# Kernel optimization log

Hardware: AMD Instinct MI355X
Metric: run time of the kernel (lower is better)

The kernel has to match this reference:

```python
import jax, jax.numpy as jnp
import numpy as np

EPS_CLAMP = 1e-6
TAU2 = 1.0


def _l2norm_rows(x):
    # F.normalize(x, p=2, dim=1) with eps=1e-12
    n = jnp.sqrt(jnp.sum(x * x, axis=1, keepdims=True))
    return x / jnp.maximum(n, 1e-12)


def _ws_v22(x_mean, x_std):
    m = _l2norm_rows(x_mean)                      # [N, F]
    c = _l2norm_rows(jnp.exp(x_std))              # [N, F]
    sq = jnp.sum(m * m, axis=1)                   # [N]
    # squared euclidean pairwise distance (cdist(...)**2)
    d2 = jnp.maximum(sq[:, None] + sq[None, :] - 2.0 * (m @ m.T), 0.0)
    csum = jnp.sum(c, axis=1)                     # [N]
    cs = jnp.sqrt(c)
    res = d2 + csum[:, None] + csum[None, :] - 2.0 * (cs @ cs.T)
    return jnp.exp(-res)                          # [N, N]


def _gcn_conv_dense(A, x, W, b):
    # PyG GCNConv with dense weighted adjacency A (A[i,j] = weight of edge i->j),
    # add_remaining_self_loops(fill=1), deg over target (column sums),
    # norm_ij = d_i^-1/2 * A_ij * d_j^-1/2, aggregate at target: out = A_norm^T @ (xW) + b
    diag = jnp.diagonal(A)
    A = A + jnp.diag(jnp.where(diag > 0, 0.0, 1.0))  # add self-loop weight 1 only where missing
    deg = jnp.sum(A, axis=0)                         # column sums (target degree)
    dis = jnp.where(deg > 0, deg ** -0.5, 0.0)
    An = dis[:, None] * A * dis[None, :]
    return An.T @ (x @ W) + b


def _encoder(A, x, W0, b0, W1, b1):
    h = jax.nn.relu(_gcn_conv_dense(A, x, W0, b0))
    return jax.nn.relu(_gcn_conv_dense(A, h, W1, b1))


def setup_inputs() -> dict:
    key = jax.random.key(0)
    ks = jax.random.split(key, 16)
    N, F, H = 4096, 512, 256
    s_in = 1.0 / np.sqrt(F)
    s_h = 1.0 / np.sqrt(2 * H)
    inp = {
        "x": jax.random.normal(ks[0], (N, F), dtype=jnp.float32),
        "new_edge": jax.random.uniform(ks[1], (N, N), dtype=jnp.float32),
        "beta": jax.random.uniform(ks[2], (1,), dtype=jnp.float32),
        "delta": jax.random.uniform(ks[3], (1,), dtype=jnp.float32),
        "eps": jax.random.uniform(ks[4], (N, N), dtype=jnp.float32),
        "Wm": jax.random.uniform(ks[5], (F, F), jnp.float32, -s_in, s_in),
        "bm": jax.random.uniform(ks[6], (F,), jnp.float32, -s_in, s_in),
        "Ws": jax.random.uniform(ks[7], (F, F), jnp.float32, -s_in, s_in),
        "bs": jax.random.uniform(ks[8], (F,), jnp.float32, -s_in, s_in),
        "mW0": jax.random.uniform(ks[9], (F, 2 * H), jnp.float32, -s_in, s_in) ,
        "mb0": jnp.zeros((2 * H,), jnp.float32),
        "mW1": jax.random.uniform(ks[10], (2 * H, H), jnp.float32, -s_h, s_h),
        "mb1": jnp.zeros((H,), jnp.float32),
        "sW0": jax.random.uniform(ks[11], (F, 2 * H), jnp.float32, -s_in, s_in),
        "sb0": jnp.zeros((2 * H,), jnp.float32),
        "sW1": jax.random.uniform(ks[12], (2 * H, H), jnp.float32, -s_h, s_h),
        "sb1": jnp.zeros((H,), jnp.float32),
    }
    return inp


def reference(x, new_edge, beta, delta, eps, Wm, bm, Ws, bs,
              mW0, mb0, mW1, mb1, sW0, sb0, sW1, sb1):
    b = beta[0]
    d = delta[0]
    x_mean = x @ Wm + bm
    x_std = x @ Ws + bs
    ws = _l2norm_rows(_ws_v22(x_mean, x_std))       # F.normalize(WS_v22(...)) row-wise
    term = (1.0 - b) * ws + b * new_edge
    term = jnp.clip(term, EPS_CLAMP, 1.0 - EPS_CLAMP)
    term = jnp.log(term / (1.0 - term))
    e = jnp.clip(eps, EPS_CLAMP, 1.0 - EPS_CLAMP)
    term = term + jnp.log(e / (1.0 - e))
    term = jax.nn.sigmoid(term / TAU2)
    term = jnp.where(term > d, term, 0.0)           # dense sparsified adjacency
    z_mean = _encoder(term, x_mean, mW0, mb0, mW1, mb1)
    z_std = _encoder(term, x_std, sW0, sb0, sW1, sb1)
    return z_mean, z_std
```

## Files before the change

### kernel.cpp

```cpp
#include <hip/hip_runtime.h>
#include <cstddef>

static constexpr int kN = 4096;
static constexpr int kF = 512;
static constexpr int kH = 256;
static constexpr float kClamp = 1e-6f;

using bf16x8 = __attribute__((ext_vector_type(8))) __bf16;
using f32x4 = __attribute__((ext_vector_type(4))) float;
using ushort8 = __attribute__((ext_vector_type(8))) unsigned short;
using ushort4v = __attribute__((ext_vector_type(4))) unsigned short;

static constexpr size_t PLANE_XF = (size_t)kN * kF;
static constexpr size_t PLANE_NN = (size_t)kN * kN;
static constexpr size_t PLANE_W = (size_t)512 * 512;
static constexpr size_t PLANE_W1 = (size_t)256 * 512;
static constexpr size_t PLANE_V0 = (size_t)1024 * kN;
static constexpr size_t PLANE_H = (size_t)kN * 1024;
static constexpr size_t PLANE_V1 = (size_t)512 * kN;

__device__ __forceinline__ unsigned short f2bf(float x) {
  unsigned int u = __float_as_uint(x);
  u += 0x7fffu + ((u >> 16) & 1u);
  return (unsigned short)(u >> 16);
}
__device__ __forceinline__ float bf2f(unsigned short h) {
  return __uint_as_float(((unsigned int)h) << 16);
}
__device__ __forceinline__ void split3(float x, unsigned short& h,
                                       unsigned short& m, unsigned short& l) {
  h = f2bf(x);
  const float r1 = x - bf2f(h);
  m = f2bf(r1);
  l = f2bf(r1 - bf2f(m));
}
__device__ __forceinline__ void split2(float x, unsigned short& h,
                                       unsigned short& m) {
  h = f2bf(x);
  m = f2bf(x - bf2f(h));
}
__device__ __forceinline__ void split2x4(const float4 v, ushort4v& h4,
                                         ushort4v& m4) {
  unsigned short h, m;
  split2(v.x, h, m); h4.x = h; m4.x = m;
  split2(v.y, h, m); h4.y = h; m4.y = m;
  split2(v.z, h, m); h4.z = h; m4.z = m;
  split2(v.w, h, m); h4.w = h; m4.w = m;
}

__device__ __forceinline__ bf16x8 ldfrag(const unsigned short* p) {
  ushort8 r = *(const ushort8*)p;
  return __builtin_bit_cast(bf16x8, r);
}
__device__ __forceinline__ f32x4 mfma16(bf16x8 a, bf16x8 b, f32x4 c) {
  return __builtin_amdgcn_mfma_f32_16x16x32_bf16(a, b, c, 0, 0, 0);
}
__device__ __forceinline__ f32x4 mfma_split6(const bf16x8* a3, const bf16x8* b3,
                                             f32x4 acc) {
  acc = mfma16(a3[2], b3[0], acc);
  acc = mfma16(a3[0], b3[2], acc);
  acc = mfma16(a3[1], b3[1], acc);
  acc = mfma16(a3[1], b3[0], acc);
  acc = mfma16(a3[0], b3[1], acc);
  acc = mfma16(a3[0], b3[0], acc);
  return acc;
}

__device__ __forceinline__ void gload16(const unsigned short* g,
                                        unsigned short* l) {
  __builtin_amdgcn_global_load_lds(
      (const __attribute__((address_space(1))) void*)g,
      (__attribute__((address_space(3))) void*)l, 16, 0, 0);
}

__device__ __forceinline__ void tri_map(int b, int& bi, int& bj) {
  int x = (int)((sqrtf(8.0f * (float)b + 1.0f) - 1.0f) * 0.5f);
  while ((x + 1) * (x + 2) / 2 <= b) ++x;
  while (x * (x + 1) / 2 > b) --x;
  bi = x;
  bj = b - x * (x + 1) / 2;
}

__device__ __forceinline__ float block_reduce_sum(float v, float* sbuf) {
  const int tid = threadIdx.x;
  sbuf[tid] = v;
  __syncthreads();
#pragma unroll
  for (int s = 128; s > 0; s >>= 1) {
    if (tid < s) sbuf[tid] += sbuf[tid + s];
    __syncthreads();
  }
  const float r = sbuf[0];
  __syncthreads();
  return r;
}

__global__ __launch_bounds__(256) void prep_w(
    const float* s0, const float* s1, const float* s2, const float* s3,
    const float* s4, const float* s5, unsigned short* d0, unsigned short* d1,
    unsigned short* d2, unsigned short* d3, unsigned short* d4,
    unsigned short* d5) {
  const int seg = blockIdx.y;
  const float* src;
  unsigned short* dst;
  int N;
  bool tri;
  switch (seg) {
    case 0: src = s0; dst = d0; N = 512; tri = true; break;
    case 1: src = s1; dst = d1; N = 512; tri = true; break;
    case 2: src = s2; dst = d2; N = 512; tri = false; break;
    case 3: src = s3; dst = d3; N = 512; tri = false; break;
    case 4: src = s4; dst = d4; N = 256; tri = false; break;
    default: src = s5; dst = d5; N = 256; tri = false; break;
  }
  const int id = blockIdx.x * 256 + threadIdx.x;
  if (id >= 512 * N) return;
  const int k = id & 511;
  const int n = id >> 9;
  const float v = src[(size_t)k * N + n];
  const size_t base = (size_t)n * 512 + k;
  const size_t plane = (size_t)512 * N;
  if (tri) {
    unsigned short h, m, l;
    split3(v, h, m, l);
    dst[base] = h;
    dst[plane + base] = m;
    dst[2 * plane + base] = l;
  } else {
    unsigned short h, m;
    split2(v, h, m);
    dst[base] = h;
    dst[plane + base] = m;
  }
}

__global__ __launch_bounds__(256) void split_x(const float* __restrict__ x,
                                               unsigned short* __restrict__ x3) {
  const size_t id = (size_t)blockIdx.x * 256 + threadIdx.x;
  unsigned short h, m, l;
  split3(x[id], h, m, l);
  x3[id] = h;
  x3[PLANE_XF + id] = m;
  x3[2 * PLANE_XF + id] = l;
}

__global__ __launch_bounds__(256) void gemm_x(
    const unsigned short* __restrict__ A3, const unsigned short* __restrict__ B30,
    const unsigned short* __restrict__ B31, float* __restrict__ C0,
    float* __restrict__ C1, const float* __restrict__ bias0,
    const float* __restrict__ bias1) {
  constexpr int BM = 128, BN = 128, K = 512;
  __shared__ __align__(16) unsigned short Asl[3][BM][40];
  __shared__ __align__(16) unsigned short Bsl[3][BN][40];
  const int tid = threadIdx.x;
  const int lane = tid & 63;
  const int wave = tid >> 6;
  const int wm = wave >> 1, wn = wave & 1;
  const int m0 = blockIdx.y * BM;
  const int n0 = blockIdx.x * BN;
  const bool str1 = (n0 >= 512);
  const int nloc = str1 ? (n0 - 512) : n0;
  const unsigned short* Bb = str1 ? B31 : B30;
  const float* bias = str1 ? bias1 : bias0;
  float* C = str1 ? C1 : C0;
  const int rl = lane & 15;
  const int kq = (lane >> 4) * 8;
  const int q = lane >> 4;

  f32x4 acc[4][4];
#pragma unroll
  for (int i = 0; i < 4; ++i)
#pragma unroll
    for (int j = 0; j < 4; ++j) acc[i][j] = (f32x4){0.f, 0.f, 0.f, 0.f};

  for (int k0 = 0; k0 < K; k0 += 32) {
#pragma unroll
    for (int it = 0; it < 6; ++it) {
      const int c = tid + it * 256;
      const int plane = c >> 9;
      const int rem = c & 511;
      const int row = rem >> 2;
      const int kc = (rem & 3) * 8;
      const ushort8 v = *(const ushort8*)(&A3[(size_t)plane * PLANE_XF +
                                              (size_t)(m0 + row) * K + k0 + kc]);
      *(ushort8*)(&Asl[plane][row][kc]) = v;
    }
#pragma unroll
    for (int it = 0; it < 6; ++it) {
      const int c = tid + it * 256;
      const int plane = c >> 9;
      const int rem = c & 511;
      const int row = rem >> 2;
      const int kc = (rem & 3) * 8;
      const ushort8 v = *(const ushort8*)(&Bb[(size_t)plane * PLANE_W +
                                              (size_t)(nloc + row) * K + k0 + kc]);
      *(ushort8*)(&Bsl[plane][row][kc]) = v;
    }
    __syncthreads();
    bf16x8 af[4][3];
#pragma unroll
    for (int mt = 0; mt < 4; ++mt)
#pragma unroll
      for (int t = 0; t < 3; ++t)
        af[mt][t] = ldfrag(&Asl[t][wm * 64 + mt * 16 + rl][kq]);
#pragma unroll
    for (int nt = 0; nt < 4; ++nt) {
      bf16x8 b3[3];
#pragma unroll
      for (int t = 0; t < 3; ++t)
        b3[t] = ldfrag(&Bsl[t][wn * 64 + nt * 16 + rl][kq]);
#pragma unroll
      for (int mt = 0; mt < 4; ++mt)
        acc[mt][nt] = mfma_split6(af[mt], b3, acc[mt][nt]);
    }
    __syncthreads();
  }
#pragma unroll
  for (int mt = 0; mt < 4; ++mt)
#pragma unroll
    for (int nt = 0; nt < 4; ++nt) {
      const int col = nloc + wn * 64 + nt * 16 + rl;
      const int row0 = m0 + wm * 64 + mt * 16 + q * 4;
      const float bv = bias[col];
#pragma unroll
      for (int r = 0; r < 4; ++r)
        C[(size_t)(row0 + r) * 512 + col] = acc[mt][nt][r] + bv;
    }
}

template <int BM, int BN>
__global__ __launch_bounds__(256) void gemm2ct(
    const unsigned short* __restrict__ A0, const unsigned short* __restrict__ A1,
    int lda, size_t planeA, const unsigned short* __restrict__ B0,
    const unsigned short* __restrict__ B1, int ldb, size_t planeB,
    unsigned short* __restrict__ Cs0, unsigned short* __restrict__ Cs1, int ldc,
    size_t planeC, int N1, int K, const float* __restrict__ rowScale) {
  __shared__ __align__(16) unsigned short Asl[2][BM][40];
  __shared__ __align__(16) unsigned short Bsl[2][BN][40];
  const int tid = threadIdx.x;
  const int lane = tid & 63;
  const int wave = tid >> 6;
  const int wm = wave >> 1, wn = wave & 1;
  const int m0 = blockIdx.y * BM;
  const int n0 = blockIdx.x * BN;
  const bool str1 = (n0 >= N1);
  const int nloc = str1 ? (n0 - N1) : n0;
  const unsigned short* Ab = str1 ? A1 : A0;
  const unsigned short* Bb = str1 ? B1 : B0;
  const int rl = lane & 15;
  const int kq = (lane >> 4) * 8;
  const int q = lane >> 4;
  constexpr int MT = BM / 32;
  constexpr int NT = BN / 32;

  f32x4 acc[MT][NT];
#pragma unroll
  for (int i = 0; i < MT; ++i)
#pragma unroll
    for (int j = 0; j < NT; ++j) acc[i][j] = (f32x4){0.f, 0.f, 0.f, 0.f};

  for (int k0 = 0; k0 < K; k0 += 32) {
    constexpr int AIT = (2 * BM * 4) / 256;
#pragma unroll
    for (int it = 0; it < AIT; ++it) {
      const int c = tid + it * 256;
      const int plane = c / (BM * 4);
      const int rem = c % (BM * 4);
      const int row = rem >> 2;
      const int kc = (rem & 3) * 8;
      const ushort8 v = *(const ushort8*)(&Ab[(size_t)plane * planeA +
                                              (size_t)(m0 + row) * lda + k0 + kc]);
      *(ushort8*)(&Asl[plane][row][kc]) = v;
    }
    constexpr int BIT = (2 * BN * 4) / 256;
#pragma unroll
    for (int it = 0; it < BIT; ++it) {
      const int c = tid + it * 256;
      const int plane = c / (BN * 4);
      const int rem = c % (BN * 4);
      const int row = rem >> 2;
      const int kc = (rem & 3) * 8;
      const ushort8 v = *(const ushort8*)(&Bb[(size_t)plane * planeB +
                                              (size_t)(nloc + row) * ldb + k0 + kc]);
      *(ushort8*)(&Bsl[plane][row][kc]) = v;
    }
    __syncthreads();
    bf16x8 af[MT][2];
#pragma unroll
    for (int mt = 0; mt < MT; ++mt)
#pragma unroll
      for (int t = 0; t < 2; ++t)
        af[mt][t] = ldfrag(&Asl[t][wm * (BM / 2) + mt * 16 + rl][kq]);
#pragma unroll
    for (int nt = 0; nt < NT; ++nt) {
      const bf16x8 b0 = ldfrag(&Bsl[0][wn * (BN / 2) + nt * 16 + rl][kq]);
      const bf16x8 b1 = ldfrag(&Bsl[1][wn * (BN / 2) + nt * 16 + rl][kq]);
#pragma unroll
      for (int mt = 0; mt < MT; ++mt) {
        acc[mt][nt] = mfma16(af[mt][1], b0, acc[mt][nt]);
        acc[mt][nt] = mfma16(af[mt][0], b1, acc[mt][nt]);
        acc[mt][nt] = mfma16(af[mt][0], b0, acc[mt][nt]);
      }
    }
    __syncthreads();
  }

#pragma unroll
  for (int mt = 0; mt < MT; ++mt) {
#pragma unroll
    for (int nt = 0; nt < NT; ++nt) {
      const int colL = nloc + wn * (BN / 2) + nt * 16 + rl;
      const int row0 = m0 + wm * (BM / 2) + mt * 16 + q * 4;
      float4 v4;
      float* vp = &v4.x;
#pragma unroll
      for (int r = 0; r < 4; ++r) {
        float v = acc[mt][nt][r];
        if (rowScale) v *= rowScale[row0 + r];
        vp[r] = v;
      }
      unsigned short* C = str1 ? Cs1 : Cs0;
      ushort4v h4, m4;
      split2x4(v4, h4, m4);
      const size_t base = (size_t)colL * ldc + row0;
      *(ushort4v*)(&C[base]) = h4;
      *(ushort4v*)(&C[planeC + base]) = m4;
    }
  }
}

template <int BM, int BN, int GX, int GYP, int GZ>
__global__ __launch_bounds__(256) void gemm2k(
    const unsigned short* __restrict__ A, int lda, size_t planeA,
    const unsigned short* __restrict__ B, int ldb, size_t planeB,
    float* __restrict__ Cp, int ldc, int Mtot, int Ksl) {
  static_assert(BM == 128 && BN == 128, "DMA staging assumes 128x128");
  __shared__ __align__(16) unsigned short Asl[2][BM][32];
  __shared__ __align__(16) unsigned short Bsl[2][BN][32];
  const int lin = blockIdx.x;
  const int xcd = lin & 7;
  const int s = lin >> 3;
  constexpr int per = GX * GYP;
  const int z = s / per;
  const int r = s - z * per;
  const int bx = r % GX;
  const int by = xcd * GYP + r / GX;
  const int m0 = by * BM;
  const int n0 = bx * BN;
  const int kOff = z * Ksl;

  const int tid = threadIdx.x;
  const int lane = tid & 63;
  const int wave = tid >> 6;
  const int wm = wave >> 1, wn = wave & 1;
  const int rl = lane & 15;
  const int kq = (lane >> 4) * 8;
  const int q = lane >> 4;
  const int kqs = kq ^ (((rl >> 1) & 3) << 3);
  const int sslot = (((lane & 3) ^ ((lane >> 3) & 3)) * 8);
  constexpr int MT = BM / 32;
  constexpr int NT = BN / 32;

  f32x4 acc[MT][NT];
#pragma unroll
  for (int i = 0; i < MT; ++i)
#pragma unroll
    for (int j = 0; j < NT; ++j) acc[i][j] = (f32x4){0.f, 0.f, 0.f, 0.f};

  for (int k0 = 0; k0 < Ksl; k0 += 32) {
#pragma unroll
    for (int it = 0; it < 8; ++it) {
      const int c = it * 4 + wave;
      const bool isB = c >= 16;
      const int cl = isB ? (c - 16) : c;
      const int pl = cl >> 3;
      const int row = (cl & 7) * 16 + (lane >> 2);
      const unsigned short* src =
          (isB ? B + (size_t)pl * planeB + (size_t)(n0 + row) * ldb
               : A + (size_t)pl * planeA + (size_t)(m0 + row) * lda) +
          kOff + k0 + sslot;
      unsigned short* dst =
          (isB ? &Bsl[0][0][0] : &Asl[0][0][0]) + cl * 512 + 0;
      gload16(src, dst);
    }
    __syncthreads();
    bf16x8 af[MT][2];
#pragma unroll
    for (int mt = 0; mt < MT; ++mt)
#pragma unroll
      for (int t = 0; t < 2; ++t)
        af[mt][t] = ldfrag(&Asl[t][wm * (BM / 2) + mt * 16 + rl][kqs]);
#pragma unroll
    for (int nt = 0; nt < NT; ++nt) {
      const bf16x8 b0 = ldfrag(&Bsl[0][wn * (BN / 2) + nt * 16 + rl][kqs]);
      const bf16x8 b1 = ldfrag(&Bsl[1][wn * (BN / 2) + nt * 16 + rl][kqs]);
#pragma unroll
      for (int mt = 0; mt < MT; ++mt) {
        acc[mt][nt] = mfma16(af[mt][1], b0, acc[mt][nt]);
        acc[mt][nt] = mfma16(af[mt][0], b1, acc[mt][nt]);
        acc[mt][nt] = mfma16(af[mt][0], b0, acc[mt][nt]);
      }
    }
    __syncthreads();
  }

  const size_t zoff = (size_t)z * (size_t)Mtot * (size_t)ldc;
#pragma unroll
  for (int mt = 0; mt < MT; ++mt) {
#pragma unroll
    for (int nt = 0; nt < NT; ++nt) {
      const int colL = n0 + wn * (BN / 2) + nt * 16 + rl;
      const int row0 = m0 + wm * (BM / 2) + mt * 16 + q * 4;
#pragma unroll
      for (int r2 = 0; r2 < 4; ++r2)
        Cp[zoff + (size_t)(row0 + r2) * ldc + colL] = acc[mt][nt][r2];
    }
  }
}

__global__ __launch_bounds__(256) void row_stats(
    const float* __restrict__ XMf, const float* __restrict__ XSf,
    unsigned short* __restrict__ M2, unsigned short* __restrict__ CS2,
    unsigned short* __restrict__ XM2, unsigned short* __restrict__ XS2,
    float* __restrict__ sq, float* __restrict__ csum) {
  __shared__ float sbuf[256];
  const int i = blockIdx.x;
  const int tid = threadIdx.x;
  const size_t base = (size_t)i * kF;
  const size_t i0 = base + tid, i1 = base + tid + 256;
  const float x0 = XMf[i0], x1 = XMf[i1];
  {
    unsigned short h, m;
    split2(x0, h, m);
    XM2[i0] = h; XM2[PLANE_XF + i0] = m;
    split2(x1, h, m);
    XM2[i1] = h; XM2[PLANE_XF + i1] = m;
  }
  const float nrm = block_reduce_sum(x0 * x0 + x1 * x1, sbuf);
  const float inv = 1.0f / fmaxf(sqrtf(nrm), 1e-12f);
  const float m0 = x0 * inv, m1 = x1 * inv;
  {
    unsigned short h, m;
    split2(m0, h, m);
    M2[i0] = h; M2[PLANE_XF + i0] = m;
    split2(m1, h, m);
    M2[i1] = h; M2[PLANE_XF + i1] = m;
  }
  const float s2 = block_reduce_sum(m0 * m0 + m1 * m1, sbuf);
  if (tid == 0) sq[i] = s2;

  const float y0 = XSf[i0], y1 = XSf[i1];
  {
    unsigned short h, m;
    split2(y0, h, m);
    XS2[i0] = h; XS2[PLANE_XF + i0] = m;
    split2(y1, h, m);
    XS2[i1] = h; XS2[PLANE_XF + i1] = m;
  }
  const float e0 = expf(y0), e1 = expf(y1);
  const float nrm2 = block_reduce_sum(e0 * e0 + e1 * e1, sbuf);
  const float inv2 = 1.0f / fmaxf(sqrtf(nrm2), 1e-12f);
  const float c0 = e0 * inv2, c1 = e1 * inv2;
  const float sc = block_reduce_sum(c0 + c1, sbuf);
  if (tid == 0) csum[i] = sc;
  {
    unsigned short h, m;
    split2(sqrtf(c0), h, m);
    CS2[i0] = h; CS2[PLANE_XF + i0] = m;
    split2(sqrtf(c1), h, m);
    CS2[i1] = h; CS2[PLANE_XF + i1] = m;
  }
}

__global__ __launch_bounds__(256) void ws_mfma2(
    const unsigned short* __restrict__ M2, const unsigned short* __restrict__ CS2,
    const float* __restrict__ sq, const float* __restrict__ csum,
    float* __restrict__ WSR) {
  __shared__ __align__(16) unsigned short S[4][2][128][40];
  int bi, bj;
  tri_map(blockIdx.x, bi, bj);
  const int i0 = bi * 128, j0 = bj * 128;
  const int tid = threadIdx.x;
  const int lane = tid & 63;
  const int wave = tid >> 6;
  const int wm = wave >> 1, wn = wave & 1;
  const int rl = lane & 15;
  const int kq = (lane >> 4) * 8;
  const int q = lane >> 4;

  f32x4 aM[4][4], aC[4][4];
#pragma unroll
  for (int i = 0; i < 4; ++i)
#pragma unroll
    for (int j = 0; j < 4; ++j) {
      aM[i][j] = (f32x4){0.f, 0.f, 0.f, 0.f};
      aC[i][j] = (f32x4){0.f, 0.f, 0.f, 0.f};
    }

  for (int k0 = 0; k0 < kF; k0 += 32) {
#pragma unroll
    for (int it = 0; it < 16; ++it) {
      const int c = tid + it * 256;
      const int op = c >> 10;
      const int rem = c & 1023;
      const int plane = rem >> 9;
      const int r2 = rem & 511;
      const int row = r2 >> 2;
      const int kc = (r2 & 3) * 8;
      const unsigned short* mat = (op & 1) ? CS2 : M2;
      const int rowoff = (op < 2) ? i0 : j0;
      const ushort8 v = *(const ushort8*)(&mat[(size_t)plane * PLANE_XF +
                                               (size_t)(rowoff + row) * kF + k0 +
                                               kc]);
      *(ushort8*)(&S[op][plane][row][kc]) = v;
    }
    __syncthreads();
    bf16x8 am[4][2], ac[4][2];
#pragma unroll
    for (int mt = 0; mt < 4; ++mt)
#pragma unroll
      for (int t = 0; t < 2; ++t) {
        am[mt][t] = ldfrag(&S[0][t][wm * 64 + mt * 16 + rl][kq]);
        ac[mt][t] = ldfrag(&S[1][t][wm * 64 + mt * 16 + rl][kq]);
      }
#pragma unroll
    for (int nt = 0; nt < 4; ++nt) {
      const bf16x8 bm0 = ldfrag(&S[2][0][wn * 64 + nt * 16 + rl][kq]);
      const bf16x8 bm1 = ldfrag(&S[2][1][wn * 64 + nt * 16 + rl][kq]);
      const bf16x8 bc0 = ldfrag(&S[3][0][wn * 64 + nt * 16 + rl][kq]);
      const bf16x8 bc1 = ldfrag(&S[3][1][wn * 64 + nt * 16 + rl][kq]);
#pragma unroll
      for (int mt = 0; mt < 4; ++mt) {
        aM[mt][nt] = mfma16(am[mt][1], bm0, aM[mt][nt]);
        aM[mt][nt] = mfma16(am[mt][0], bm1, aM[mt][nt]);
        aM[mt][nt] = mfma16(am[mt][0], bm0, aM[mt][nt]);
        aC[mt][nt] = mfma16(ac[mt][1], bc0, aC[mt][nt]);
        aC[mt][nt] = mfma16(ac[mt][0], bc1, aC[mt][nt]);
        aC[mt][nt] = mfma16(ac[mt][0], bc0, aC[mt][nt]);
      }
    }
    __syncthreads();
  }

#pragma unroll
  for (int mt = 0; mt < 4; ++mt) {
#pragma unroll
    for (int nt = 0; nt < 4; ++nt) {
      const int j = j0 + wn * 64 + nt * 16 + rl;
      const int ib = i0 + wm * 64 + mt * 16 + q * 4;
      const float sqj = sq[j], csj = csum[j];
      float4 vv;
      float* vp = &vv.x;
#pragma unroll
      for (int r = 0; r < 4; ++r) {
        const int i = ib + r;
        const float d2 = fmaxf(sq[i] + sqj - 2.0f * aM[mt][nt][r], 0.0f);
        const float res = d2 + csum[i] + csj - 2.0f * aC[mt][nt][r];
        const float v = expf(-res);
        vp[r] = v;
        WSR[(size_t)i * kN + j] = v;
      }
      if (bi != bj) *(float4*)(&WSR[(size_t)j * kN + ib]) = vv;
    }
  }
}

__global__ __launch_bounds__(256) void row_invnorm_kernel(
    const float* __restrict__ WSR, float* __restrict__ invn) {
  __shared__ float sbuf[256];
  const int i = blockIdx.x;
  const int tid = threadIdx.x;
  const float4* rp = (const float4*)(WSR + (size_t)i * kN);
  float s = 0.0f;
#pragma unroll
  for (int q = 0; q < (kN / 4) / 256; ++q) {
    const float4 v = rp[tid + q * 256];
    s += v.x * v.x + v.y * v.y + v.z * v.z + v.w * v.w;
  }
  s = block_reduce_sum(s, sbuf);
  if (tid == 0) invn[i] = 1.0f / fmaxf(sqrtf(s), 1e-12f);
}

__device__ __forceinline__ float adj_val(float w, float inv, float nev, float ev,
                                         float b, float d, bool diag) {
  float t = (1.0f - b) * (w * inv) + b * nev;
  t = fminf(fmaxf(t, kClamp), 1.0f - kClamp);
  float L = logf(t / (1.0f - t));
  const float e = fminf(fmaxf(ev, kClamp), 1.0f - kClamp);
  L += logf(e / (1.0f - e));
  const float s = 1.0f / (1.0f + expf(-L));
  float v = (s > d) ? s : 0.0f;
  if (diag) v = (v > 0.0f) ? v : 1.0f;
  return v;
}

__global__ __launch_bounds__(256) void adj_transpose(
    const float* __restrict__ WSR, const float* __restrict__ invn,
    const float* __restrict__ ne, const float* __restrict__ epsm,
    const float* __restrict__ beta_p, const float* __restrict__ delta_p,
    unsigned short* __restrict__ Adj2, float* __restrict__ degp) {
  __shared__ float T0[64][65];
  __shared__ float T1[64][65];
  const float b = beta_p[0];
  const float d = delta_p[0];
  int bi, bj;
  tri_map(blockIdx.x, bi, bj);
  const int i0 = bi * 64, j0 = bj * 64;
  const int tid = threadIdx.x;
  const int rlq = tid >> 4;
  const int cq = (tid & 15) * 4;
#pragma unroll
  for (int p = 0; p < 4; ++p) {
    const int ii = p * 16 + rlq;
    {
      const size_t off = (size_t)(i0 + ii) * kN + j0 + cq;
      const float4 w4 = *(const float4*)(&WSR[off]);
      const float4 n4 = *(const float4*)(&ne[off]);
      const float4 e4 = *(const float4*)(&epsm[off]);
      const float inv = invn[i0 + ii];
      const float wv[4] = {w4.x, w4.y, w4.z, w4.w};
      const float nv[4] = {n4.x, n4.y, n4.z, n4.w};
      const float ev[4] = {e4.x, e4.y, e4.z, e4.w};
#pragma unroll
      for (int u = 0; u < 4; ++u)
        T0[ii][cq + u] =
            adj_val(wv[u], inv, nv[u], ev[u], b, d, (i0 + ii) == (j0 + cq + u));
    }
    if (bi != bj) {
      const size_t off = (size_t)(j0 + ii) * kN + i0 + cq;
      const float4 w4 = *(const float4*)(&WSR[off]);
      const float4 n4 = *(const float4*)(&ne[off]);
      const float4 e4 = *(const float4*)(&epsm[off]);
      const float inv = invn[j0 + ii];
      const float wv[4] = {w4.x, w4.y, w4.z, w4.w};
      const float nv[4] = {n4.x, n4.y, n4.z, n4.w};
      const float ev[4] = {e4.x, e4.y, e4.z, e4.w};
#pragma unroll
      for (int u = 0; u < 4; ++u)
        T1[ii][cq + u] = adj_val(wv[u], inv, nv[u], ev[u], b, d, false);
    }
  }
  __syncthreads();
#pragma unroll
  for (int p = 0; p < 4; ++p) {
    const int jj = p * 16 + rlq;
    {
      const float4 v4 = make_float4(T0[cq + 0][jj], T0[cq + 1][jj],
                                    T0[cq + 2][jj], T0[cq + 3][jj]);
      ushort4v h4, m4;
      split2x4(v4, h4, m4);
      const size_t base = (size_t)(j0 + jj) * kN + i0 + cq;
      *(ushort4v*)(&Adj2[base]) = h4;
      *(ushort4v*)(&Adj2[PLANE_NN + base]) = m4;
    }
    if (bi != bj) {
      const float4 v4 = make_float4(T1[cq + 0][jj], T1[cq + 1][jj],
                                    T1[cq + 2][jj], T1[cq + 3][jj]);
      ushort4v h4, m4;
      split2x4(v4, h4, m4);
      const size_t base = (size_t)(i0 + jj) * kN + j0 + cq;
      *(ushort4v*)(&Adj2[base]) = h4;
      *(ushort4v*)(&Adj2[PLANE_NN + base]) = m4;
    }
  }
  if (tid < 64) {
    float s = 0.0f;
#pragma unroll 8
    for (int ii = 0; ii < 64; ++ii) s += T0[ii][tid];
    degp[(size_t)bi * kN + j0 + tid] = s;
    if (bi != bj) {
      float s1 = 0.0f;
#pragma unroll 8
      for (int ii = 0; ii < 64; ++ii) s1 += T1[ii][tid];
      degp[(size_t)bj * kN + i0 + tid] = s1;
    }
  }
}

__global__ __launch_bounds__(256) void deg_dis_kernel(
    const float* __restrict__ degp, float* __restrict__ dis) {
  const int j = blockIdx.x * 256 + threadIdx.x;
  float s = 0.0f;
#pragma unroll
  for (int c = 0; c < 64; ++c) s += degp[(size_t)c * kN + j];
  dis[j] = (s > 0.0f) ? (1.0f / sqrtf(s)) : 0.0f;
}

__global__ __launch_bounds__(256) void combine_h(
    const float* __restrict__ hp, const float* __restrict__ dis,
    const float* __restrict__ b0, const float* __restrict__ b1,
    unsigned short* __restrict__ h2) {
  const size_t qd = (size_t)blockIdx.x * 256 + threadIdx.x;
  const int m = (int)(qd >> 8);
  const int c0 = (int)(qd & 255) * 4;
  const size_t off = (size_t)m * 1024 + c0;
  const float4 s0 = *(const float4*)(&hp[off]);
  const float4 s1 = *(const float4*)(&hp[PLANE_H + off]);
  const float4 s2 = *(const float4*)(&hp[2 * PLANE_H + off]);
  const float4 s3 = *(const float4*)(&hp[3 * PLANE_H + off]);
  const float4 bv = (c0 < 512) ? *(const float4*)(&b0[c0])
                               : *(const float4*)(&b1[c0 - 512]);
  const float ds = dis[m];
  float4 v4;
  v4.x = fmaxf(ds * (s0.x + s1.x + s2.x + s3.x) + bv.x, 0.f);
  v4.y = fmaxf(ds * (s0.y + s1.y + s2.y + s3.y) + bv.y, 0.f);
  v4.z = fmaxf(ds * (s0.z + s1.z + s2.z + s3.z) + bv.z, 0.f);
  v4.w = fmaxf(ds * (s0.w + s1.w + s2.w + s3.w) + bv.w, 0.f);
  ushort4v h4, m4;
  split2x4(v4, h4, m4);
  *(ushort4v*)(&h2[off]) = h4;
  *(ushort4v*)(&h2[PLANE_H + off]) = m4;
}

__global__ __launch_bounds__(256) void combine_z(
    const float* __restrict__ zp, const float* __restrict__ dis,
    const float* __restrict__ b0, const float* __restrict__ b1,
    float* __restrict__ out) {
  const size_t qd = (size_t)blockIdx.x * 256 + threadIdx.x;
  const int m = (int)(qd >> 7);
  const int c0 = (int)(qd & 127) * 4;
  const size_t off = (size_t)m * 512 + c0;
  constexpr size_t PZ = (size_t)kN * 512;
  const float4 s0 = *(const float4*)(&zp[off]);
  const float4 s1 = *(const float4*)(&zp[PZ + off]);
  const float4 s2 = *(const float4*)(&zp[2 * PZ + off]);
  const float4 s3 = *(const float4*)(&zp[3 * PZ + off]);
  const float4 bv = (c0 < 256) ? *(const float4*)(&b0[c0])
                               : *(const float4*)(&b1[c0 - 256]);
  const float ds = dis[m];
  float4 v4;
  v4.x = fmaxf(ds * (s0.x + s1.x + s2.x + s3.x) + bv.x, 0.f);
  v4.y = fmaxf(ds * (s0.y + s1.y + s2.y + s3.y) + bv.y, 0.f);
  v4.z = fmaxf(ds * (s0.z + s1.z + s2.z + s3.z) + bv.z, 0.f);
  v4.w = fmaxf(ds * (s0.w + s1.w + s2.w + s3.w) + bv.w, 0.f);
  float* dst = (c0 < 256) ? &out[(size_t)m * 256 + c0]
                          : &out[(size_t)kN * 256 + (size_t)m * 256 + (c0 - 256)];
  *(float4*)dst = v4;
}

extern "C" void kernel_launch(void* const* d_in, const int* in_sizes, int n_in,
                              void* d_out, int out_size, void* d_ws,
                              size_t ws_size, hipStream_t stream) {
  const float* x = (const float*)d_in[0];
  const float* ne = (const float*)d_in[1];
  const float* beta = (const float*)d_in[2];
  const float* delta = (const float*)d_in[3];
  const float* epsm = (const float*)d_in[4];
  const float* Wm = (const float*)d_in[5];
  const float* bm = (const float*)d_in[6];
  const float* Ws = (const float*)d_in[7];
  const float* bs = (const float*)d_in[8];
  const float* mW0 = (const float*)d_in[9];
  const float* mb0 = (const float*)d_in[10];
  const float* mW1 = (const float*)d_in[11];
  const float* mb1 = (const float*)d_in[12];
  const float* sW0 = (const float*)d_in[13];
  const float* sb0 = (const float*)d_in[14];
  const float* sW1 = (const float*)d_in[15];
  const float* sb1 = (const float*)d_in[16];
  float* out = (float*)d_out;

  char* p = (char*)d_ws;
  float* WSR = (float*)p;                     p += PLANE_NN * 4;
  unsigned short* Adj2 = (unsigned short*)p;  p += 2 * PLANE_NN * 2;
  unsigned short* x3 = (unsigned short*)p;    p += 3 * PLANE_XF * 2;
  float* XMf = (float*)p;                     p += PLANE_XF * 4;
  float* XSf = (float*)p;                     p += PLANE_XF * 4;
  unsigned short* XM2 = (unsigned short*)p;   p += 2 * PLANE_XF * 2;
  unsigned short* XS2 = (unsigned short*)p;   p += 2 * PLANE_XF * 2;
  unsigned short* M2 = (unsigned short*)p;    p += 2 * PLANE_XF * 2;
  unsigned short* CS2 = (unsigned short*)p;   p += 2 * PLANE_XF * 2;
  unsigned short* Wm3 = (unsigned short*)p;   p += 3 * PLANE_W * 2;
  unsigned short* Ws3 = (unsigned short*)p;   p += 3 * PLANE_W * 2;
  unsigned short* mW0t2 = (unsigned short*)p; p += 2 * PLANE_W * 2;
  unsigned short* sW0t2 = (unsigned short*)p; p += 2 * PLANE_W * 2;
  unsigned short* mW1t2 = (unsigned short*)p; p += 2 * PLANE_W1 * 2;
  unsigned short* sW1t2 = (unsigned short*)p; p += 2 * PLANE_W1 * 2;
  float* degp = (float*)p;                    p += (size_t)64 * kN * 4;
  float* sq = (float*)p;                      p += kN * 4;
  float* csum = (float*)p;                    p += kN * 4;
  float* invn = (float*)p;                    p += kN * 4;
  float* dis = (float*)p;                     p += kN * 4;

  float* hp = WSR;
  float* zp = WSR;
  unsigned short* V1t2 = x3;
  unsigned short* h2 = XM2;
  unsigned short* V0t2 = M2;

  const dim3 blk(256);
  const int nTri = (kN / 64) * (kN / 64 + 1) / 2;
  const int nTri128 = (kN / 128) * (kN / 128 + 1) / 2;

  prep_w<<<dim3(1024, 6), blk, 0, stream>>>(Wm, Ws, mW0, sW0, mW1, sW1, Wm3,
                                            Ws3, mW0t2, sW0t2, mW1t2, sW1t2);
  split_x<<<(kN * kF) / 256, blk, 0, stream>>>(x, x3);

  gemm_x<<<dim3(8, 32), blk, 0, stream>>>(x3, Wm3, Ws3, XMf, XSf, bm, bs);

  row_stats<<<kN, blk, 0, stream>>>(XMf, XSf, M2, CS2, XM2, XS2, sq, csum);

  ws_mfma2<<<nTri128, blk, 0, stream>>>(M2, CS2, sq, csum, WSR);

  row_invnorm_kernel<<<kN, blk, 0, stream>>>(WSR, invn);

  adj_transpose<<<nTri, blk, 0, stream>>>(WSR, invn, ne, epsm, beta, delta,
                                          Adj2, degp);
  deg_dis_kernel<<<kN / 256, blk, 0, stream>>>(degp, dis);

  gemm2ct<128, 64><<<dim3(16, 32), blk, 0, stream>>>(
      XM2, XS2, kF, PLANE_XF, mW0t2, sW0t2, kF, PLANE_W, V0t2,
      V0t2 + (size_t)512 * kN, kN, PLANE_V0, 512, kF, dis);

  gemm2k<128, 128, 8, 4, 4><<<1024, blk, 0, stream>>>(
      Adj2, kN, PLANE_NN, V0t2, kN, PLANE_V0, hp, 1024, kN, kN / 4);
  combine_h<<<(int)(PLANE_H / 4 / 256), blk, 0, stream>>>(hp, dis, mb0, sb0, h2);

  gemm2ct<64, 64><<<dim3(8, 64), blk, 0, stream>>>(
      h2, h2 + 512, 1024, PLANE_H, mW1t2, sW1t2, kF, PLANE_W1, V1t2,
      V1t2 + (size_t)256 * kN, kN, PLANE_V1, 256, kF, dis);

  gemm2k<128, 128, 4, 4, 4><<<512, blk, 0, stream>>>(
      Adj2, kN, PLANE_NN, V1t2, kN, PLANE_V1, zp, 512, kN, kN / 4);
  combine_z<<<(int)((size_t)kN * 512 / 4 / 256), blk, 0, stream>>>(zp, dis, mb1,
                                                                   sb1, out);
}
```

Measured before the change: 691.5 us.

## Simplify logit-sigmoid algebra, swizzle direct-to-LDS loads in ws_mfma2, shrink gemm_x tile

The adjacency value is rewritten so that sigmoid(logit(t)+logit(e)) becomes t·e / (t·e + (1−t)(1−e)). This removes two logs, an exp and extra divides per N×N element. ws_mfma2 now loads tiles with gload16 (global-to-LDS) into an unpadded, XOR-swizzled shared layout and requests two blocks per CU via launch bounds. gemm_x uses 128×64 tiles with twice as many blocks to improve CU coverage, at the cost of less data reuse per block. The algebraic form can round differently near the delta threshold and when the clamp is active.

Measured after the change: 605.4 us. -12.5%, faster.

```diff
diff --git a/kernel.cpp b/kernel.cpp
--- a/kernel.cpp
+++ b/kernel.cpp
@@ -149,7 +149,7 @@
     const unsigned short* __restrict__ B31, float* __restrict__ C0,
     float* __restrict__ C1, const float* __restrict__ bias0,
     const float* __restrict__ bias1) {
-  constexpr int BM = 128, BN = 128, K = 512;
+  constexpr int BM = 128, BN = 64, K = 512;
   __shared__ __align__(16) unsigned short Asl[3][BM][40];
   __shared__ __align__(16) unsigned short Bsl[3][BN][40];
   const int tid = threadIdx.x;
@@ -167,18 +167,18 @@
   const int kq = (lane >> 4) * 8;
   const int q = lane >> 4;
 
-  f32x4 acc[4][4];
+  f32x4 acc[4][2];
 #pragma unroll
   for (int i = 0; i < 4; ++i)
 #pragma unroll
-    for (int j = 0; j < 4; ++j) acc[i][j] = (f32x4){0.f, 0.f, 0.f, 0.f};
+    for (int j = 0; j < 2; ++j) acc[i][j] = (f32x4){0.f, 0.f, 0.f, 0.f};
 
   for (int k0 = 0; k0 < K; k0 += 32) {
 #pragma unroll
     for (int it = 0; it < 6; ++it) {
       const int c = tid + it * 256;
-      const int plane = c >> 9;
-      const int rem = c & 511;
+      const int plane = c / (BM * 4);
+      const int rem = c % (BM * 4);
       const int row = rem >> 2;
       const int kc = (rem & 3) * 8;
       const ushort8 v = *(const ushort8*)(&A3[(size_t)plane * PLANE_XF +
@@ -186,10 +186,10 @@
       *(ushort8*)(&Asl[plane][row][kc]) = v;
     }
 #pragma unroll
-    for (int it = 0; it < 6; ++it) {
+    for (int it = 0; it < 3; ++it) {
       const int c = tid + it * 256;
-      const int plane = c >> 9;
-      const int rem = c & 511;
+      const int plane = c / (BN * 4);
+      const int rem = c % (BN * 4);
       const int row = rem >> 2;
       const int kc = (rem & 3) * 8;
       const ushort8 v = *(const ushort8*)(&Bb[(size_t)plane * PLANE_W +
@@ -197,29 +197,29 @@
       *(ushort8*)(&Bsl[plane][row][kc]) = v;
     }
     __syncthreads();
-    bf16x8 af[4][3];
+    bf16x8 af[4][3], bfr[2][3];
 #pragma unroll
     for (int mt = 0; mt < 4; ++mt)
 #pragma unroll
       for (int t = 0; t < 3; ++t)
         af[mt][t] = ldfrag(&Asl[t][wm * 64 + mt * 16 + rl][kq]);
 #pragma unroll
-    for (int nt = 0; nt < 4; ++nt) {
-      bf16x8 b3[3];
+    for (int nt = 0; nt < 2; ++nt)
 #pragma unroll
       for (int t = 0; t < 3; ++t)
-        b3[t] = ldfrag(&Bsl[t][wn * 64 + nt * 16 + rl][kq]);
-#pragma unroll
-      for (int mt = 0; mt < 4; ++mt)
-        acc[mt][nt] = mfma_split6(af[mt], b3, acc[mt][nt]);
-    }
+        bfr[nt][t] = ldfrag(&Bsl[t][wn * 32 + nt * 16 + rl][kq]);
+#pragma unroll
+    for (int mt = 0; mt < 4; ++mt)
+#pragma unroll
+      for (int nt = 0; nt < 2; ++nt)
+        acc[mt][nt] = mfma_split6(af[mt], bfr[nt], acc[mt][nt]);
     __syncthreads();
   }
 #pragma unroll
   for (int mt = 0; mt < 4; ++mt)
 #pragma unroll
-    for (int nt = 0; nt < 4; ++nt) {
-      const int col = nloc + wn * 64 + nt * 16 + rl;
+    for (int nt = 0; nt < 2; ++nt) {
+      const int col = nloc + wn * 32 + nt * 16 + rl;
       const int row0 = m0 + wm * 64 + mt * 16 + q * 4;
       const float bv = bias[col];
 #pragma unroll
@@ -472,11 +472,11 @@
   }
 }
 
-__global__ __launch_bounds__(256) void ws_mfma2(
+__global__ __launch_bounds__(256, 2) void ws_mfma2(
     const unsigned short* __restrict__ M2, const unsigned short* __restrict__ CS2,
     const float* __restrict__ sq, const float* __restrict__ csum,
     float* __restrict__ WSR) {
-  __shared__ __align__(16) unsigned short S[4][2][128][40];
+  __shared__ __align__(16) unsigned short S[4][2][128][32];
   int bi, bj;
   tri_map(blockIdx.x, bi, bj);
   const int i0 = bi * 128, j0 = bj * 128;
@@ -487,6 +487,8 @@
   const int rl = lane & 15;
   const int kq = (lane >> 4) * 8;
   const int q = lane >> 4;
+  const int kqs = kq ^ (((rl >> 1) & 3) << 3);
+  const int sslot = (((lane & 3) ^ ((lane >> 3) & 3)) * 8);
 
   f32x4 aM[4][4], aC[4][4];
 #pragma unroll
@@ -500,19 +502,16 @@
   for (int k0 = 0; k0 < kF; k0 += 32) {
 #pragma unroll
     for (int it = 0; it < 16; ++it) {
-      const int c = tid + it * 256;
-      const int op = c >> 10;
-      const int rem = c & 1023;
-      const int plane = rem >> 9;
-      const int r2 = rem & 511;
-      const int row = r2 >> 2;
-      const int kc = (r2 & 3) * 8;
+      const int c = it * 4 + wave;
+      const int op = c >> 4;
+      const int plane = (c >> 3) & 1;
+      const int row = (c & 7) * 16 + (lane >> 2);
       const unsigned short* mat = (op & 1) ? CS2 : M2;
       const int rowoff = (op < 2) ? i0 : j0;
-      const ushort8 v = *(const ushort8*)(&mat[(size_t)plane * PLANE_XF +
-                                               (size_t)(rowoff + row) * kF + k0 +
-                                               kc]);
-      *(ushort8*)(&S[op][plane][row][kc]) = v;
+      const unsigned short* src = mat + (size_t)plane * PLANE_XF +
+                                  (size_t)(rowoff + row) * kF + k0 + sslot;
+      unsigned short* dst = &S[0][0][0][0] + c * 512;
+      gload16(src, dst);
     }
     __syncthreads();
     bf16x8 am[4][2], ac[4][2];
@@ -520,15 +519,15 @@
     for (int mt = 0; mt < 4; ++mt)
 #pragma unroll
       for (int t = 0; t < 2; ++t) {
-        am[mt][t] = ldfrag(&S[0][t][wm * 64 + mt * 16 + rl][kq]);
-        ac[mt][t] = ldfrag(&S[1][t][wm * 64 + mt * 16 + rl][kq]);
+        am[mt][t] = ldfrag(&S[0][t][wm * 64 + mt * 16 + rl][kqs]);
+        ac[mt][t] = ldfrag(&S[1][t][wm * 64 + mt * 16 + rl][kqs]);
       }
 #pragma unroll
     for (int nt = 0; nt < 4; ++nt) {
-      const bf16x8 bm0 = ldfrag(&S[2][0][wn * 64 + nt * 16 + rl][kq]);
-      const bf16x8 bm1 = ldfrag(&S[2][1][wn * 64 + nt * 16 + rl][kq]);
-      const bf16x8 bc0 = ldfrag(&S[3][0][wn * 64 + nt * 16 + rl][kq]);
-      const bf16x8 bc1 = ldfrag(&S[3][1][wn * 64 + nt * 16 + rl][kq]);
+      const bf16x8 bm0 = ldfrag(&S[2][0][wn * 64 + nt * 16 + rl][kqs]);
+      const bf16x8 bm1 = ldfrag(&S[2][1][wn * 64 + nt * 16 + rl][kqs]);
+      const bf16x8 bc0 = ldfrag(&S[3][0][wn * 64 + nt * 16 + rl][kqs]);
+      const bf16x8 bc1 = ldfrag(&S[3][1][wn * 64 + nt * 16 + rl][kqs]);
 #pragma unroll
       for (int mt = 0; mt < 4; ++mt) {
         aM[mt][nt] = mfma16(am[mt][1], bm0, aM[mt][nt]);
@@ -585,10 +584,10 @@
                                          float b, float d, bool diag) {
   float t = (1.0f - b) * (w * inv) + b * nev;
   t = fminf(fmaxf(t, kClamp), 1.0f - kClamp);
-  float L = logf(t / (1.0f - t));
   const float e = fminf(fmaxf(ev, kClamp), 1.0f - kClamp);
-  L += logf(e / (1.0f - e));
-  const float s = 1.0f / (1.0f + expf(-L));
+  const float num = t * e;
+  const float den = num + (1.0f - t) * (1.0f - e);
+  const float s = num / den;
   float v = (s > d) ? s : 0.0f;
   if (diag) v = (v > 0.0f) ? v : 1.0f;
   return v;
@@ -796,7 +795,7 @@
                                             Ws3, mW0t2, sW0t2, mW1t2, sW1t2);
   split_x<<<(kN * kF) / 256, blk, 0, stream>>>(x, x3);
 
-  gemm_x<<<dim3(8, 32), blk, 0, stream>>>(x3, Wm3, Ws3, XMf, XSf, bm, bs);
+  gemm_x<<<dim3(16, 32), blk, 0, stream>>>(x3, Wm3, Ws3, XMf, XSf, bm, bs);
 
   row_stats<<<kN, blk, 0, stream>>>(XMf, XSf, M2, CS2, XM2, XS2, sq, csum);
 
```
